# Kernel tuning notes

Measured on AMD Instinct MI355X. Metric: run time of the kernel, lower is better.

The kernel has to match this reference:

```python
import jax, jax.numpy as jnp
import numpy as np

B, C, H, W = 8, 512, 64, 64
TEMB = 512
HIDDEN = 1024  # int(C * prompt_hidden_ratio=2.0)
K = C // 2     # max(1, int(C * topk_ratio=0.5))


def silu(x):
    return x * jax.nn.sigmoid(x)


def conv1x1(h, w, b):
    # h: [b,c,hh,ww], w: [out,in], b: [out]
    return jnp.einsum('bchw,oc->bohw', h, w) + b[None, :, None, None]


def setup_inputs() -> dict:
    key = jax.random.key(0)
    ks = jax.random.split(key, 12)
    s = 0.02  # small init so softmax/attention stay well-conditioned
    return {
        'x': jax.random.normal(ks[0], (B, C, H, W), jnp.float32),
        'temb': jax.random.normal(ks[1], (B, TEMB), jnp.float32),
        'w_affine': jax.random.normal(ks[2], (2 * C, TEMB), jnp.float32) * s,
        'b_affine': jnp.zeros((2 * C,), jnp.float32),
        'w_tp': jax.random.normal(ks[3], (C, TEMB), jnp.float32) * s,
        'b_tp': jnp.zeros((C,), jnp.float32),
        'w_m1': jax.random.normal(ks[4], (HIDDEN, 2 * C), jnp.float32) * s,
        'b_m1': jnp.zeros((HIDDEN,), jnp.float32),
        'w_m2': jax.random.normal(ks[5], (C, HIDDEN), jnp.float32) * s,
        'b_m2': jnp.zeros((C,), jnp.float32),
        'wq': jax.random.normal(ks[6], (C, C), jnp.float32) * s,
        'bq': jnp.zeros((C,), jnp.float32),
        'wk': jax.random.normal(ks[7], (C, C), jnp.float32) * s,
        'bk': jnp.zeros((C,), jnp.float32),
        'wv': jax.random.normal(ks[8], (C, C), jnp.float32) * s,
        'bv': jnp.zeros((C,), jnp.float32),
        'wo': jax.random.normal(ks[9], (C, C), jnp.float32) * s,
        'bo': jnp.zeros((C,), jnp.float32),
    }


def reference(x, temb, w_affine, b_affine, w_tp, b_tp, w_m1, b_m1, w_m2, b_m2,
              wq, bq, wk, bk, wv, bv, wo, bo):
    b, c, hgt, wgt = x.shape
    hw = hgt * wgt

    # TimeScaleShift
    temb_act = silu(temb)
    ss = temb_act @ w_affine.T + b_affine              # [b, 2c]
    scale, shift = jnp.split(ss, 2, axis=1)
    h = x * (1.0 + scale[:, :, None, None]) + shift[:, :, None, None]

    # channel prompt
    gap = h.mean(axis=(2, 3))                          # [b, c]
    time_prompt = temb_act @ w_tp.T + b_tp             # [b, c]
    pm = jnp.concatenate([gap, time_prompt], axis=1)   # [b, 2c]
    prompt = silu(pm @ w_m1.T + b_m1) @ w_m2.T + b_m2  # [b, c]

    # top-k channel selection
    _, topk_idx = jax.lax.top_k(prompt, K)             # [b, K] int32

    # q/k/v 1x1 convs, then gather selected channels
    qf = conv1x1(h, wq, bq).reshape(b, c, hw)
    kf = conv1x1(h, wk, bk).reshape(b, c, hw)
    vf = conv1x1(h, wv, bv).reshape(b, c, hw)
    idx3 = topk_idx[:, :, None]
    q = jnp.take_along_axis(qf, idx3, axis=1)          # [b, K, hw]
    k_feat = jnp.take_along_axis(kf, idx3, axis=1)
    v = jnp.take_along_axis(vf, idx3, axis=1)

    # channel attention on the selected subset
    attn = jnp.einsum('bkn,bln->bkl', q, k_feat) * (K ** -0.5)  # [b, K, K]
    attn = jax.nn.softmax(attn, axis=2)
    out = jnp.einsum('bkl,bln->bkn', attn, v)                   # [b, K, hw]

    # scatter back into a zero tensor at the selected channels
    out_full = jax.vmap(
        lambda o, i: jnp.zeros((c, hw), o.dtype).at[i].set(o)
    )(out, topk_idx).reshape(b, c, hgt, wgt)

    return conv1x1(out_full, wo, bo)
```

## Files before the change

### kernel.cpp

```cpp
#include <hip/hip_runtime.h>
#include <hip/hip_bf16.h>
#include <math.h>

typedef __hip_bfloat16 bf16;
typedef __bf16 bf16x8 __attribute__((ext_vector_type(8)));
typedef float f32x4 __attribute__((ext_vector_type(4)));

static __device__ __forceinline__ float b2f(bf16 v) { return __bfloat162float(v); }
static __device__ __forceinline__ bf16 f2b(float v) { return __float2bfloat16(v); }

#define TM 128
#define TN 64
#define TK 32

template <typename TOUT>
__global__ __launch_bounds__(256) void gemm_bt(
    const bf16* __restrict__ A, size_t sA,
    const bf16* __restrict__ Bt, size_t sB,
    const float* __restrict__ bias, size_t sBias, int hasBias,
    TOUT* __restrict__ D, size_t sD,
    int M, int N, int Kd, int transStore)
{
    A  += (size_t)blockIdx.z * sA;
    Bt += (size_t)blockIdx.z * sB;
    D  += (size_t)blockIdx.z * sD;
    if (hasBias) bias += (size_t)blockIdx.z * sBias;

    const int m0 = blockIdx.y * TM, n0 = blockIdx.x * TN;
    const int t = threadIdx.x, wv = t >> 6, lane = t & 63;
    const int lr = lane & 15, quad = lane >> 4;

    __shared__ bf16 lA[TM][TK + 8];
    __shared__ bf16 lB[TN][TK + 8];

    f32x4 acc[2][4];
#pragma unroll
    for (int i = 0; i < 2; ++i)
#pragma unroll
        for (int j = 0; j < 4; ++j) acc[i][j] = (f32x4){0.f, 0.f, 0.f, 0.f};

    const int arow = t >> 1, acol = (t & 1) * 16;
    const int brow = t >> 2, bcol = (t & 3) * 8;
    const bf16* aptr = A  + (size_t)(m0 + arow) * Kd + acol;
    const bf16* bptr = Bt + (size_t)(n0 + brow) * Kd + bcol;

    for (int k0 = 0; k0 < Kd; k0 += TK) {
        __syncthreads();
        uint4 a0 = *(const uint4*)(aptr + k0);
        uint4 a1 = *(const uint4*)(aptr + k0 + 8);
        uint4 b0 = *(const uint4*)(bptr + k0);
        *(uint4*)(&lA[arow][acol])     = a0;
        *(uint4*)(&lA[arow][acol + 8]) = a1;
        *(uint4*)(&lB[brow][bcol])     = b0;
        __syncthreads();

        bf16x8 af0 = *(const bf16x8*)(&lA[wv * 32 + lr][quad * 8]);
        bf16x8 af1 = *(const bf16x8*)(&lA[wv * 32 + 16 + lr][quad * 8]);
#pragma unroll
        for (int j = 0; j < 4; ++j) {
            bf16x8 bfj = *(const bf16x8*)(&lB[j * 16 + lr][quad * 8]);
            acc[0][j] = __builtin_amdgcn_mfma_f32_16x16x32_bf16(af0, bfj, acc[0][j], 0, 0, 0);
            acc[1][j] = __builtin_amdgcn_mfma_f32_16x16x32_bf16(af1, bfj, acc[1][j], 0, 0, 0);
        }
    }

#pragma unroll
    for (int i = 0; i < 2; ++i) {
        const int mb = m0 + wv * 32 + i * 16 + quad * 4;
#pragma unroll
        for (int r = 0; r < 4; ++r) {
            const int mm = mb + r;
            const float bvv = hasBias ? bias[mm] : 0.f;
#pragma unroll
            for (int j = 0; j < 4; ++j) {
                const int nn = n0 + j * 16 + lr;
                const float v = acc[i][j][r] + bvv;
                const size_t o = transStore ? ((size_t)nn * M + mm)
                                            : ((size_t)mm * N + nn);
                if constexpr (__is_same(TOUT, float)) D[o] = v;
                else                                  D[o] = f2b(v);
            }
        }
    }
}

__global__ __launch_bounds__(256) void gemm_qkv(
    const bf16* __restrict__ Aall, const bf16* __restrict__ hT,
    const float* __restrict__ bias,
    bf16* __restrict__ qb, bf16* __restrict__ kb, bf16* __restrict__ vT)
{
    const int b = blockIdx.z;
    const int m0 = blockIdx.y * 128;
    const int n0 = blockIdx.x * 64;
    const bf16* A  = Aall + (size_t)b * 393216;
    const bf16* Bt = hT   + (size_t)b * 2097152;
    bias += b * 768;

    const int t = threadIdx.x, wv = t >> 6, lane = t & 63;
    const int lr = lane & 15, quad = lane >> 4;

    __shared__ bf16 lA[3][128][TK + 8];
    __shared__ bf16 lB[64][TK + 8];

    f32x4 acc[3][2][4];
#pragma unroll
    for (int m = 0; m < 3; ++m)
#pragma unroll
        for (int i = 0; i < 2; ++i)
#pragma unroll
            for (int j = 0; j < 4; ++j) acc[m][i][j] = (f32x4){0.f, 0.f, 0.f, 0.f};

    const int arow = t >> 1, acol = (t & 1) * 16;
    const int brow = t >> 2, bcol = (t & 3) * 8;
    const bf16* aptr = A  + (size_t)(m0 + arow) * 512 + acol;
    const bf16* bptr = Bt + (size_t)(n0 + brow) * 512 + bcol;

    for (int k0 = 0; k0 < 512; k0 += TK) {
        __syncthreads();
        uint4 a[3][2], b0;
#pragma unroll
        for (int m = 0; m < 3; ++m) {
            a[m][0] = *(const uint4*)(aptr + m * 131072 + k0);
            a[m][1] = *(const uint4*)(aptr + m * 131072 + k0 + 8);
        }
        b0 = *(const uint4*)(bptr + k0);
#pragma unroll
        for (int m = 0; m < 3; ++m) {
            *(uint4*)(&lA[m][arow][acol])     = a[m][0];
            *(uint4*)(&lA[m][arow][acol + 8]) = a[m][1];
        }
        *(uint4*)(&lB[brow][bcol]) = b0;
        __syncthreads();

        bf16x8 af[3][2];
#pragma unroll
        for (int m = 0; m < 3; ++m) {
            af[m][0] = *(const bf16x8*)(&lA[m][wv * 32 + lr][quad * 8]);
            af[m][1] = *(const bf16x8*)(&lA[m][wv * 32 + 16 + lr][quad * 8]);
        }
#pragma unroll
        for (int j = 0; j < 4; ++j) {
            bf16x8 bfj = *(const bf16x8*)(&lB[j * 16 + lr][quad * 8]);
#pragma unroll
            for (int m = 0; m < 3; ++m) {
                acc[m][0][j] = __builtin_amdgcn_mfma_f32_16x16x32_bf16(af[m][0], bfj, acc[m][0][j], 0, 0, 0);
                acc[m][1][j] = __builtin_amdgcn_mfma_f32_16x16x32_bf16(af[m][1], bfj, acc[m][1][j], 0, 0, 0);
            }
        }
    }

#pragma unroll
    for (int m = 0; m < 3; ++m) {
#pragma unroll
        for (int i = 0; i < 2; ++i) {
            const int mb = m0 + wv * 32 + i * 16 + quad * 4;
#pragma unroll
            for (int r = 0; r < 4; ++r) {
                const int mm = mb + r;
                const float bvv = bias[m * 256 + mm];
#pragma unroll
                for (int j = 0; j < 4; ++j) {
                    const int nn = n0 + j * 16 + lr;
                    const float v = acc[m][i][j][r] + bvv;
                    if (m == 0)      qb[(size_t)b * 1048576 + (size_t)mm * 4096 + nn] = f2b(v);
                    else if (m == 1) kb[(size_t)b * 1048576 + (size_t)mm * 4096 + nn] = f2b(v);
                    else             vT[(size_t)b * 1048576 + (size_t)nn * 256 + mm] = f2b(v);
                }
            }
        }
    }
}

__global__ __launch_bounds__(256) void gemm_s_splitk(
    const bf16* __restrict__ qb, const bf16* __restrict__ kb,
    float* __restrict__ part)
{
    const int b = blockIdx.z >> 4, s = blockIdx.z & 15;
    const int m0 = blockIdx.y * TM, n0 = blockIdx.x * TN;
    const bf16* A  = qb + (size_t)b * 1048576;
    const bf16* Bt = kb + (size_t)b * 1048576;

    const int t = threadIdx.x, wv = t >> 6, lane = t & 63;
    const int lr = lane & 15, quad = lane >> 4;

    __shared__ bf16 lA[TM][TK + 8];
    __shared__ bf16 lB[TN][TK + 8];

    f32x4 acc[2][4];
#pragma unroll
    for (int i = 0; i < 2; ++i)
#pragma unroll
        for (int j = 0; j < 4; ++j) acc[i][j] = (f32x4){0.f, 0.f, 0.f, 0.f};

    const int arow = t >> 1, acol = (t & 1) * 16;
    const int brow = t >> 2, bcol = (t & 3) * 8;
    const bf16* aptr = A  + (size_t)(m0 + arow) * 4096 + acol;
    const bf16* bptr = Bt + (size_t)(n0 + brow) * 4096 + bcol;

    const int kBeg = s * 256, kEnd = kBeg + 256;
    for (int k0 = kBeg; k0 < kEnd; k0 += TK) {
        __syncthreads();
        uint4 a0 = *(const uint4*)(aptr + k0);
        uint4 a1 = *(const uint4*)(aptr + k0 + 8);
        uint4 b0 = *(const uint4*)(bptr + k0);
        *(uint4*)(&lA[arow][acol])     = a0;
        *(uint4*)(&lA[arow][acol + 8]) = a1;
        *(uint4*)(&lB[brow][bcol])     = b0;
        __syncthreads();

        bf16x8 af0 = *(const bf16x8*)(&lA[wv * 32 + lr][quad * 8]);
        bf16x8 af1 = *(const bf16x8*)(&lA[wv * 32 + 16 + lr][quad * 8]);
#pragma unroll
        for (int j = 0; j < 4; ++j) {
            bf16x8 bfj = *(const bf16x8*)(&lB[j * 16 + lr][quad * 8]);
            acc[0][j] = __builtin_amdgcn_mfma_f32_16x16x32_bf16(af0, bfj, acc[0][j], 0, 0, 0);
            acc[1][j] = __builtin_amdgcn_mfma_f32_16x16x32_bf16(af1, bfj, acc[1][j], 0, 0, 0);
        }
    }

    float* dst = part + ((size_t)(s * 8 + b) * 256) * 256;
#pragma unroll
    for (int i = 0; i < 2; ++i) {
        const int mb = m0 + wv * 32 + i * 16 + quad * 4;
#pragma unroll
        for (int r = 0; r < 4; ++r) {
            const int mm = mb + r;
#pragma unroll
            for (int j = 0; j < 4; ++j)
                dst[(size_t)mm * 256 + n0 + j * 16 + lr] = acc[i][j][r];
        }
    }
}


__global__ void k_silu(const float* __restrict__ in, float* __restrict__ out, int n)
{
    int i = blockIdx.x * 256 + threadIdx.x;
    if (i < n) {
        float v = in[i];
        out[i] = v / (1.f + expf(-v));
    }
}

__global__ void k_smallgemm(const float* __restrict__ in, const float* __restrict__ W,
                            const float* __restrict__ bias, float* __restrict__ out,
                            int Mrows, int O, int Kd, int act)
{
    const int gw = (blockIdx.x * 256 + threadIdx.x) >> 6;
    const int lane = threadIdx.x & 63;
    if (gw >= Mrows * O) return;
    const int m = gw / O, o = gw - m * O;
    float s = 0.f;
    for (int k = lane; k < Kd; k += 64)
        s += in[m * Kd + k] * W[(size_t)o * Kd + k];
    for (int off = 32; off; off >>= 1) s += __shfl_down(s, off);
    if (lane == 0) {
        s += bias[o];
        if (act) s = s / (1.f + expf(-s));
        out[m * O + o] = s;
    }
}

__global__ void k_mlp1(const float* __restrict__ ss, const float* __restrict__ xsum,
                       const float* __restrict__ tp, const float* __restrict__ w_m1,
                       const float* __restrict__ b_m1, float* __restrict__ hidden)
{
    const int gw = (blockIdx.x * 256 + threadIdx.x) >> 6;
    const int lane = threadIdx.x & 63;
    if (gw >= 8 * 1024) return;
    const int m = gw >> 10, o = gw & 1023;
    float s = 0.f;
    for (int k = lane; k < 1024; k += 64) {
        float pv;
        if (k < 512) pv = (1.f + ss[m * 1024 + k]) * (xsum[m * 512 + k] * (1.f / 4096.f))
                          + ss[m * 1024 + 512 + k];
        else         pv = tp[m * 512 + k - 512];
        s += pv * w_m1[(size_t)o * 1024 + k];
    }
    for (int off = 32; off; off >>= 1) s += __shfl_down(s, off);
    if (lane == 0) {
        s += b_m1[o];
        hidden[m * 1024 + o] = s / (1.f + expf(-s));
    }
}

__global__ void k_topk(const float* __restrict__ prompt, int* __restrict__ idx)
{
    __shared__ float v[512];
    __shared__ int sel[512];
    const int b = blockIdx.x, c = threadIdx.x;
    v[c] = prompt[b * 512 + c];
    __syncthreads();
    const float mv = v[c];
    int rank = 0;
    for (int j = 0; j < 512; ++j) {
        float o = v[j];
        rank += (o > mv) || (o == mv && j < c);
    }
    sel[c] = (rank < 256) ? 1 : 0;
    __syncthreads();
    if (rank < 256) {
        int pos = 0;
        for (int j = 0; j < c; ++j) pos += sel[j];
        idx[b * 256 + pos] = c;
    }
}

__global__ void k_hT(const float* __restrict__ x, const float* __restrict__ ss,
                     bf16* __restrict__ hT, float* __restrict__ xsum)
{
    __shared__ bf16 tile[32][33];
    const int b = blockIdx.z, c0 = blockIdx.y * 32, n0 = blockIdx.x * 32;
    const int t = threadIdx.x, tj = t & 31, ti = t >> 5;
    float rowsum[4];
#pragma unroll
    for (int r = 0; r < 4; ++r) {
        const int i = ti + r * 8;
        const int c = c0 + i;
        const float sc = 1.f + ss[b * 1024 + c];
        const float sh = ss[b * 1024 + 512 + c];
        const float xv = x[((size_t)b * 512 + c) * 4096 + n0 + tj];
        tile[i][tj] = f2b(xv * sc + sh);
        rowsum[r] = xv;
    }
#pragma unroll
    for (int r = 0; r < 4; ++r) {
        float s = rowsum[r];
        for (int off = 16; off; off >>= 1) s += __shfl_down(s, off, 32);
        if (tj == 0) atomicAdd(&xsum[b * 512 + c0 + ti + r * 8], s);
    }
    __syncthreads();
#pragma unroll
    for (int r = 0; r < 4; ++r) {
        const int j = ti + r * 8;
        hT[((size_t)b * 4096 + n0 + j) * 512 + c0 + tj] = tile[tj][j];
    }
}

__global__ void k_gather(const int* __restrict__ idx,
                         const float* __restrict__ wq, const float* __restrict__ bq,
                         const float* __restrict__ wk, const float* __restrict__ bk,
                         const float* __restrict__ wv, const float* __restrict__ bv,
                         const float* __restrict__ wo,
                         bf16* __restrict__ wqkv_g, float* __restrict__ bqkv_g,
                         bf16* __restrict__ wo_g)
{
    const int b = blockIdx.z;
    const int* id = idx + b * 256;
    const int tid = blockIdx.x * 256 + threadIdx.x;
    {
        const int mat = tid >> 17, r = tid & 131071;
        const int j = r >> 9, c = r & 511;
        const int ch = id[j];
        const float* W = mat == 0 ? wq : (mat == 1 ? wk : wv);
        wqkv_g[(size_t)b * 393216 + tid] = f2b(W[ch * 512 + c]);
    }
    if (tid < 131072) {
        const int o = tid >> 8, j = tid & 255;
        wo_g[(size_t)b * 131072 + tid] = f2b(wo[o * 512 + id[j]]);
    }
    if (tid < 768) {
        const int m2 = tid >> 8, j = tid & 255;
        const float* Bv = m2 == 0 ? bq : (m2 == 1 ? bk : bv);
        bqkv_g[b * 768 + tid] = Bv[id[j]];
    }
}

__global__ void k_softmax_red(const float* __restrict__ part, bf16* __restrict__ Pt)
{
    const int row = blockIdx.x;
    const int b = row >> 8, j = row & 255;
    const int t = threadIdx.x;
    const int lane = t & 63, wv = t >> 6;
    __shared__ float redm[4], reds[4];
    float v = 0.f;
#pragma unroll
    for (int s = 0; s < 16; ++s)
        v += part[((size_t)(s * 8 + b) * 256 + j) * 256 + t];
    v *= 0.0625f;
    float m = v;
    for (int off = 32; off; off >>= 1) m = fmaxf(m, __shfl_down(m, off));
    if (lane == 0) redm[wv] = m;
    __syncthreads();
    m = fmaxf(fmaxf(redm[0], redm[1]), fmaxf(redm[2], redm[3]));
    const float e = __expf(v - m);
    float s = e;
    for (int off = 32; off; off >>= 1) s += __shfl_down(s, off);
    if (lane == 0) reds[wv] = s;
    __syncthreads();
    s = reds[0] + reds[1] + reds[2] + reds[3];
    Pt[(size_t)b * 65536 + (size_t)t * 256 + j] = f2b(e / s);
}


extern "C" void kernel_launch(void* const* d_in, const int* in_sizes, int n_in,
                              void* d_out, int out_size, void* d_ws, size_t ws_size,
                              hipStream_t stream)
{
    const float* x        = (const float*)d_in[0];
    const float* temb     = (const float*)d_in[1];
    const float* w_affine = (const float*)d_in[2];
    const float* b_affine = (const float*)d_in[3];
    const float* w_tp     = (const float*)d_in[4];
    const float* b_tp     = (const float*)d_in[5];
    const float* w_m1     = (const float*)d_in[6];
    const float* b_m1     = (const float*)d_in[7];
    const float* w_m2     = (const float*)d_in[8];
    const float* b_m2     = (const float*)d_in[9];
    const float* wq       = (const float*)d_in[10];
    const float* bq       = (const float*)d_in[11];
    const float* wk       = (const float*)d_in[12];
    const float* bk       = (const float*)d_in[13];
    const float* wv       = (const float*)d_in[14];
    const float* bv       = (const float*)d_in[15];
    const float* wo       = (const float*)d_in[16];
    const float* bo       = (const float*)d_in[17];
    float* out = (float*)d_out;

    char* ws = (char*)d_ws;
    size_t off = 0;
    auto alloc = [&](size_t bytes) -> char* {
        char* p = ws + off;
        off += (bytes + 255) & ~(size_t)255;
        return p;
    };

    float* temb_act = (float*)alloc(4096 * 4);
    float* ssb      = (float*)alloc(8192 * 4);
    float* tp       = (float*)alloc(4096 * 4);
    float* xsum     = (float*)alloc(4096 * 4);
    float* hidden   = (float*)alloc(8192 * 4);
    float* prompt   = (float*)alloc(4096 * 4);
    int*   idx      = (int*)alloc(2048 * 4);
    char*  hT_part  = alloc((size_t)8 * 4096 * 512 * 2);
    bf16*  hT   = (bf16*)hT_part;
    float* part = (float*)hT_part;
    bf16*  wqkv_g = (bf16*)alloc((size_t)8 * 768 * 512 * 2);
    float* bqkv_g = (float*)alloc(8 * 768 * 4);
    bf16*  wo_g   = (bf16*)alloc((size_t)8 * 512 * 256 * 2);
    bf16*  qb     = (bf16*)alloc((size_t)8 * 256 * 4096 * 2);
    bf16*  kb     = (bf16*)alloc((size_t)8 * 256 * 4096 * 2);
    bf16*  vT     = (bf16*)alloc((size_t)8 * 4096 * 256 * 2);
    bf16*  Pt     = (bf16*)alloc((size_t)8 * 256 * 256 * 2);
    bf16*  W2     = (bf16*)alloc((size_t)8 * 512 * 256 * 2);
    (void)ws_size; (void)n_in; (void)in_sizes; (void)out_size;

    hipMemsetAsync(xsum, 0, 4096 * 4, stream);
    k_silu<<<16, 256, 0, stream>>>(temb, temb_act, 4096);
    k_smallgemm<<<2048, 256, 0, stream>>>(temb_act, w_affine, b_affine, ssb, 8, 1024, 512, 0);
    k_smallgemm<<<1024, 256, 0, stream>>>(temb_act, w_tp, b_tp, tp, 8, 512, 512, 0);
    k_hT<<<dim3(128, 16, 8), 256, 0, stream>>>(x, ssb, hT, xsum);
    k_mlp1<<<2048, 256, 0, stream>>>(ssb, xsum, tp, w_m1, b_m1, hidden);
    k_smallgemm<<<1024, 256, 0, stream>>>(hidden, w_m2, b_m2, prompt, 8, 512, 1024, 0);
    k_topk<<<8, 512, 0, stream>>>(prompt, idx);
    k_gather<<<dim3(1536, 1, 8), 256, 0, stream>>>(idx, wq, bq, wk, bk, wv, bv, wo,
                                                   wqkv_g, bqkv_g, wo_g);
    gemm_qkv<<<dim3(64, 2, 8), 256, 0, stream>>>(wqkv_g, hT, bqkv_g, qb, kb, vT);
    gemm_s_splitk<<<dim3(4, 2, 128), 256, 0, stream>>>(qb, kb, part);
    k_softmax_red<<<2048, 256, 0, stream>>>(part, Pt);
    gemm_bt<bf16><<<dim3(4, 4, 8), 256, 0, stream>>>(wo_g, 131072, Pt, 65536,
                                                     nullptr, 0, 0,
                                                     W2, 131072, 512, 256, 256, 0);
    gemm_bt<float><<<dim3(64, 4, 8), 256, 0, stream>>>(W2, 131072, vT, 1048576,
                                                       bo, 0, 1,
                                                       out, 2097152, 512, 4096, 256, 0);
}
```

Before: 407.9 us.

## Fuse scale-shift and transpose into QKV GEMM B-tile load, drop hT buffer

```diff
diff --git a/kernel.cpp b/kernel.cpp
--- a/kernel.cpp
+++ b/kernel.cpp
@@ -84,23 +84,24 @@
     }
 }
 
+#define BROW 40
+
 __global__ __launch_bounds__(256) void gemm_qkv(
-    const bf16* __restrict__ Aall, const bf16* __restrict__ hT,
-    const float* __restrict__ bias,
+    const bf16* __restrict__ Aall, const float* __restrict__ x,
+    const float* __restrict__ ss, const float* __restrict__ bias,
     bf16* __restrict__ qb, bf16* __restrict__ kb, bf16* __restrict__ vT)
 {
     const int b = blockIdx.z;
     const int m0 = blockIdx.y * 128;
     const int n0 = blockIdx.x * 64;
-    const bf16* A  = Aall + (size_t)b * 393216;
-    const bf16* Bt = hT   + (size_t)b * 2097152;
+    const bf16* A = Aall + (size_t)b * 393216;
     bias += b * 768;
 
     const int t = threadIdx.x, wv = t >> 6, lane = t & 63;
     const int lr = lane & 15, quad = lane >> 4;
 
     __shared__ bf16 lA[3][128][TK + 8];
-    __shared__ bf16 lB[64][TK + 8];
+    __shared__ bf16 lBf[64 * BROW];
 
     f32x4 acc[3][2][4];
 #pragma unroll
@@ -111,25 +112,39 @@
             for (int j = 0; j < 4; ++j) acc[m][i][j] = (f32x4){0.f, 0.f, 0.f, 0.f};
 
     const int arow = t >> 1, acol = (t & 1) * 16;
-    const int brow = t >> 2, bcol = (t & 3) * 8;
-    const bf16* aptr = A  + (size_t)(m0 + arow) * 512 + acol;
-    const bf16* bptr = Bt + (size_t)(n0 + brow) * 512 + bcol;
+    const bf16* aptr = A + (size_t)(m0 + arow) * 512 + acol;
+    const int kk = t >> 3;
+    const int w8 = kk >> 3;
+    const int nc = (t & 7) * 8;
+    const float* xp0 = x + ((size_t)b * 512 + kk) * 4096 + n0 + nc;
+    const float* ssp = ss + b * 1024 + kk;
 
     for (int k0 = 0; k0 < 512; k0 += TK) {
         __syncthreads();
-        uint4 a[3][2], b0;
+        uint4 a[3][2];
 #pragma unroll
         for (int m = 0; m < 3; ++m) {
             a[m][0] = *(const uint4*)(aptr + m * 131072 + k0);
             a[m][1] = *(const uint4*)(aptr + m * 131072 + k0 + 8);
         }
-        b0 = *(const uint4*)(bptr + k0);
+        const float4 f0 = *(const float4*)(xp0 + (size_t)k0 * 4096);
+        const float4 f1 = *(const float4*)(xp0 + (size_t)k0 * 4096 + 4);
+        const float sc = 1.f + ssp[k0];
+        const float sh = ssp[512 + k0];
 #pragma unroll
         for (int m = 0; m < 3; ++m) {
             *(uint4*)(&lA[m][arow][acol])     = a[m][0];
             *(uint4*)(&lA[m][arow][acol + 8]) = a[m][1];
         }
-        *(uint4*)(&lB[brow][bcol]) = b0;
+        {
+            const float vals[8] = {f0.x, f0.y, f0.z, f0.w, f1.x, f1.y, f1.z, f1.w};
+#pragma unroll
+            for (int i = 0; i < 8; ++i) {
+                const int n = nc + i;
+                lBf[n * BROW + ((w8 ^ ((n >> 3) & 3)) << 3) + (kk & 7)] =
+                    f2b(fmaf(vals[i], sc, sh));
+            }
+        }
         __syncthreads();
 
         bf16x8 af[3][2];
@@ -140,7 +155,8 @@
         }
 #pragma unroll
         for (int j = 0; j < 4; ++j) {
-            bf16x8 bfj = *(const bf16x8*)(&lB[j * 16 + lr][quad * 8]);
+            const int n = j * 16 + lr;
+            bf16x8 bfj = *(const bf16x8*)(&lBf[n * BROW + ((quad ^ ((n >> 3) & 3)) << 3)]);
 #pragma unroll
             for (int m = 0; m < 3; ++m) {
                 acc[m][0][j] = __builtin_amdgcn_mfma_f32_16x16x32_bf16(af[m][0], bfj, acc[m][0][j], 0, 0, 0);
@@ -240,6 +256,24 @@
         float v = in[i];
         out[i] = v / (1.f + expf(-v));
     }
+}
+
+__global__ void k_xmean(const float* __restrict__ x, float* __restrict__ xsum)
+{
+    const int bc = blockIdx.x;
+    const float4* p = (const float4*)(x + (size_t)bc * 4096);
+    float s = 0.f;
+#pragma unroll
+    for (int r = 0; r < 4; ++r) {
+        float4 v = p[threadIdx.x + r * 256];
+        s += v.x + v.y + v.z + v.w;
+    }
+    for (int off = 32; off; off >>= 1) s += __shfl_down(s, off);
+    __shared__ float red[4];
+    if ((threadIdx.x & 63) == 0) red[threadIdx.x >> 6] = s;
+    __syncthreads();
+    if (threadIdx.x == 0)
+        xsum[bc] = red[0] + red[1] + red[2] + red[3];
 }
 
 __global__ void k_smallgemm(const float* __restrict__ in, const float* __restrict__ W,
@@ -303,37 +337,6 @@
         int pos = 0;
         for (int j = 0; j < c; ++j) pos += sel[j];
         idx[b * 256 + pos] = c;
-    }
-}
-
-__global__ void k_hT(const float* __restrict__ x, const float* __restrict__ ss,
-                     bf16* __restrict__ hT, float* __restrict__ xsum)
-{
-    __shared__ bf16 tile[32][33];
-    const int b = blockIdx.z, c0 = blockIdx.y * 32, n0 = blockIdx.x * 32;
-    const int t = threadIdx.x, tj = t & 31, ti = t >> 5;
-    float rowsum[4];
-#pragma unroll
-    for (int r = 0; r < 4; ++r) {
-        const int i = ti + r * 8;
-        const int c = c0 + i;
-        const float sc = 1.f + ss[b * 1024 + c];
-        const float sh = ss[b * 1024 + 512 + c];
-        const float xv = x[((size_t)b * 512 + c) * 4096 + n0 + tj];
-        tile[i][tj] = f2b(xv * sc + sh);
-        rowsum[r] = xv;
-    }
-#pragma unroll
-    for (int r = 0; r < 4; ++r) {
-        float s = rowsum[r];
-        for (int off = 16; off; off >>= 1) s += __shfl_down(s, off, 32);
-        if (tj == 0) atomicAdd(&xsum[b * 512 + c0 + ti + r * 8], s);
-    }
-    __syncthreads();
-#pragma unroll
-    for (int r = 0; r < 4; ++r) {
-        const int j = ti + r * 8;
-        hT[((size_t)b * 4096 + n0 + j) * 512 + c0 + tj] = tile[tj][j];
     }
 }
 
@@ -432,9 +435,7 @@
     float* hidden   = (float*)alloc(8192 * 4);
     float* prompt   = (float*)alloc(4096 * 4);
     int*   idx      = (int*)alloc(2048 * 4);
-    char*  hT_part  = alloc((size_t)8 * 4096 * 512 * 2);
-    bf16*  hT   = (bf16*)hT_part;
-    float* part = (float*)hT_part;
+    float* part   = (float*)alloc((size_t)16 * 8 * 256 * 256 * 4);
     bf16*  wqkv_g = (bf16*)alloc((size_t)8 * 768 * 512 * 2);
     float* bqkv_g = (float*)alloc(8 * 768 * 4);
     bf16*  wo_g   = (bf16*)alloc((size_t)8 * 512 * 256 * 2);
@@ -445,17 +446,16 @@
     bf16*  W2     = (bf16*)alloc((size_t)8 * 512 * 256 * 2);
     (void)ws_size; (void)n_in; (void)in_sizes; (void)out_size;
 
-    hipMemsetAsync(xsum, 0, 4096 * 4, stream);
     k_silu<<<16, 256, 0, stream>>>(temb, temb_act, 4096);
+    k_xmean<<<4096, 256, 0, stream>>>(x, xsum);
     k_smallgemm<<<2048, 256, 0, stream>>>(temb_act, w_affine, b_affine, ssb, 8, 1024, 512, 0);
     k_smallgemm<<<1024, 256, 0, stream>>>(temb_act, w_tp, b_tp, tp, 8, 512, 512, 0);
-    k_hT<<<dim3(128, 16, 8), 256, 0, stream>>>(x, ssb, hT, xsum);
     k_mlp1<<<2048, 256, 0, stream>>>(ssb, xsum, tp, w_m1, b_m1, hidden);
     k_smallgemm<<<1024, 256, 0, stream>>>(hidden, w_m2, b_m2, prompt, 8, 512, 1024, 0);
     k_topk<<<8, 512, 0, stream>>>(prompt, idx);
     k_gather<<<dim3(1536, 1, 8), 256, 0, stream>>>(idx, wq, bq, wk, bk, wv, bv, wo,
                                                    wqkv_g, bqkv_g, wo_g);
-    gemm_qkv<<<dim3(64, 2, 8), 256, 0, stream>>>(wqkv_g, hT, bqkv_g, qb, kb, vT);
+    gemm_qkv<<<dim3(64, 2, 8), 256, 0, stream>>>(wqkv_g, x, ssb, bqkv_g, qb, kb, vT);
     gemm_s_splitk<<<dim3(4, 2, 128), 256, 0, stream>>>(qb, kb, part);
     k_softmax_red<<<2048, 256, 0, stream>>>(part, Pt);
     gemm_bt<bf16><<<dim3(4, 4, 8), 256, 0, stream>>>(wo_g, 131072, Pt, 65536,
```

Result: faster. 333.3 us (-18.3%).
